# Kernel optimization log

Measured on AMD Instinct MI355X. Metric: run time of the kernel, lower is better.

## Reference

```python
import jax, jax.numpy as jnp
import numpy as np

NUM_QUANTIZERS = 4  # num_quantizers


def setup_inputs() -> dict:
    key = jax.random.key(0)
    k1, k2 = jax.random.split(key)
    x = jax.random.normal(k1, (8, 64, 128, 128), dtype=jnp.float32)
    codebook = jax.random.normal(k2, (512, 64), dtype=jnp.float32)
    return {"x": x, "codebook": codebook}


def reference(x, codebook):
    """Residual VQ with shared Euclidean codebook, straight-through estimator.

    x: [B, C, H, W] image feature map; codebook: [K, C].
    Returns (quantized [B,C,H,W], indices [B,H,W,Q] int32, commit_loss [Q]).
    """
    B, C, H, W = x.shape
    flat = x.transpose(0, 2, 3, 1).reshape(-1, C)  # [N, C], N = B*H*W
    c_sq = jnp.sum(codebook * codebook, axis=-1)   # [K]

    residual = flat
    quant_out = jnp.zeros_like(flat)
    idx_list, losses = [], []
    for _ in range(NUM_QUANTIZERS):
        # argmin ||r - c||^2 == argmin (||c||^2 - 2 r.c); ||r||^2 constant per row
        dist = c_sq[None, :] - 2.0 * (residual @ codebook.T)  # [N, K]
        idx = jnp.argmin(dist, axis=-1)                        # [N]
        quant = codebook[idx]                                  # [N, C] gather
        # commitment loss: mse(stop_grad(quant), residual)
        losses.append(jnp.mean(jnp.square(jax.lax.stop_gradient(quant) - residual)))
        # straight-through: gradients flow to residual, not codebook
        quant_st = residual + jax.lax.stop_gradient(quant - residual)
        quant_out = quant_out + quant_st
        residual = residual - jax.lax.stop_gradient(quant)
        idx_list.append(idx)

    quantized = quant_out.reshape(B, H, W, C).transpose(0, 3, 1, 2)
    indices = jnp.stack(idx_list, axis=-1).reshape(B, H, W, NUM_QUANTIZERS)
    commit_loss = jnp.stack(losses)
    return quantized, indices, commit_loss
```

## Files before the change

### kernel.cpp

```cpp
#include <hip/hip_runtime.h>


#define NPTS   131072
#define CH     64
#define KCODE  512
#define NQ     4
#define HW     16384
#define BPTS   64
#define BTHR   256

__device__ __forceinline__ void load_lds16(const float* g, float* l) {
    __builtin_amdgcn_global_load_lds(
        (const __attribute__((address_space(1))) void*)g,
        (__attribute__((address_space(3))) void*)l, 16, 0, 0);
}

__global__ void prep_cbS(const float* __restrict__ cb, float* __restrict__ cbS) {
    int g = blockIdx.x * 256 + threadIdx.x;
    int c = g >> 9, pos = g & 511;
    int i = pos >> 7, cg = (pos >> 2) & 31, j = pos & 3;
    int k = cg * 16 + i * 4 + j;
    cbS[g] = cb[k * CH + c];
}

__global__ void prep_csq(const float* __restrict__ cb, float* __restrict__ csq) {
    int k = blockIdx.x * 256 + threadIdx.x;
    if (k < KCODE) {
        const float4* row = (const float4*)(cb + (size_t)k * CH);
        float a0 = 0.f, a1 = 0.f, a2 = 0.f, a3 = 0.f;
#pragma unroll
        for (int j = 0; j < CH / 4; ++j) {
            float4 v = row[j];
            a0 = fmaf(v.x, v.x, a0); a1 = fmaf(v.y, v.y, a1);
            a2 = fmaf(v.z, v.z, a2); a3 = fmaf(v.w, v.w, a3);
        }
        csq[k] = (a0 + a1) + (a2 + a3);
    }
}

__global__ __launch_bounds__(BTHR, 2) void rvq_main(
    const float* __restrict__ x, const float* __restrict__ cb,
    const float* __restrict__ cbS, const float* __restrict__ csq_g,
    float* __restrict__ out_quant, float* __restrict__ out_idx,
    float* __restrict__ out_loss)
{
    __shared__ __align__(16) float s_res[CH * BPTS];
    __shared__ __align__(16) float s_cb[16 * KCODE];
    __shared__ __align__(16) float s_csq[KCODE];
    __shared__ int   s_bidx[BPTS];
    __shared__ int   s_idx4[BPTS * NQ];

    float* s_rd   = s_cb;
    int*   s_ri   = (int*)(s_cb + 64 * 33);
    float* s_loss = s_cb + 2 * 64 * 33;

    const int tid  = threadIdx.x;
    const int lane = tid & 63;
    const int w    = tid >> 6;
    const int cg   = tid & 31;
    const int pg   = tid >> 5;

    const int n0  = blockIdx.x * BPTS;
    const int b   = n0 >> 14;
    const int hw0 = n0 & (HW - 1);
    const float* xbase = x + (size_t)b * CH * HW + hw0;

    for (int j = tid; j < CH * BPTS / 4; j += BTHR) {
        int c = j >> 4, p4 = j & 15;
        *(float4*)&s_res[c * BPTS + p4 * 4] =
            *(const float4*)(xbase + (size_t)c * HW + p4 * 4);
    }
    for (int j = tid; j < KCODE; j += BTHR) s_csq[j] = csq_g[j];

    float lossq[NQ], idxf[NQ];

    for (int q = 0; q < NQ; ++q) {
        float acc[8][16];
        {
            if (q == 0) { __syncthreads(); }
            const float4* cq4 = (const float4*)(s_csq + cg * 16);
            float4 c0 = cq4[0], c1 = cq4[1], c2 = cq4[2], c3 = cq4[3];
            float ci[16] = {c0.x, c0.y, c0.z, c0.w, c1.x, c1.y, c1.z, c1.w,
                            c2.x, c2.y, c2.z, c2.w, c3.x, c3.y, c3.z, c3.w};
#pragma unroll
            for (int p = 0; p < 8; ++p)
#pragma unroll
                for (int n = 0; n < 16; ++n) acc[p][n] = -0.5f * ci[n];
        }

        for (int chk = 0; chk < 4; ++chk) {
            __syncthreads();
            const float* src = cbS + chk * (16 * KCODE);
#pragma unroll
            for (int r = 0; r < 8; ++r) {
                int off = (w * 8 + r) * 256;
                load_lds16(src + off + lane * 4, s_cb + off);
            }
            __syncthreads();
#pragma unroll 2
            for (int cc = 0; cc < 16; ++cc) {
                const int c = chk * 16 + cc;
                const float* ar = &s_res[c * BPTS + pg * 8];
                float4 a0 = *(const float4*)(ar + 0);
                float4 a1 = *(const float4*)(ar + 4);
                float av[8] = {a0.x, a0.y, a0.z, a0.w, a1.x, a1.y, a1.z, a1.w};
                const float* br = &s_cb[cc * KCODE + cg * 4];
#pragma unroll
                for (int nb = 0; nb < 4; ++nb) {
                    float4 bq = *(const float4*)(br + nb * 128);
#pragma unroll
                    for (int p = 0; p < 8; ++p) {
                        acc[p][nb * 4 + 0] = fmaf(av[p], bq.x, acc[p][nb * 4 + 0]);
                        acc[p][nb * 4 + 1] = fmaf(av[p], bq.y, acc[p][nb * 4 + 1]);
                        acc[p][nb * 4 + 2] = fmaf(av[p], bq.z, acc[p][nb * 4 + 2]);
                        acc[p][nb * 4 + 3] = fmaf(av[p], bq.w, acc[p][nb * 4 + 3]);
                    }
                }
            }
        }

        float bd[8]; int bi[8];
#pragma unroll
        for (int p = 0; p < 8; ++p) {
            float B = acc[p][0]; int I = cg * 16;
#pragma unroll
            for (int n = 1; n < 16; ++n)
                if (acc[p][n] > B) { B = acc[p][n]; I = cg * 16 + n; }
            bd[p] = B; bi[p] = I;
        }

        __syncthreads();
#pragma unroll
        for (int p = 0; p < 8; ++p) {
            s_rd[(pg * 8 + p) * 33 + cg] = bd[p];
            s_ri[(pg * 8 + p) * 33 + cg] = bi[p];
        }
        __syncthreads();
        if (tid < BPTS) {
            float B = -3.4e38f; int I = 0x7fffffff;
            for (int g2 = 0; g2 < 32; ++g2) {
                float s = s_rd[tid * 33 + g2];
                int   k = s_ri[tid * 33 + g2];
                if (s > B || (s == B && k < I)) { B = s; I = k; }
            }
            idxf[q] = (float)I;
            s_bidx[tid] = I;
            s_idx4[tid * 4 + q] = I;
        }
        __syncthreads();

        {
            const int p  = tid & 63;
            const int cq = tid >> 6;
            int bix = s_bidx[p];
            const float4* crow = (const float4*)(cb + (size_t)bix * CH + cq * 16);
            float l0 = 0.f, l1 = 0.f, l2 = 0.f, l3 = 0.f;
#pragma unroll
            for (int i = 0; i < 4; ++i) {
                float4 v = crow[i];
                int c = cq * 16 + i * 4;
                float r0 = s_res[(c + 0) * BPTS + p] - v.x;
                float r1 = s_res[(c + 1) * BPTS + p] - v.y;
                float r2 = s_res[(c + 2) * BPTS + p] - v.z;
                float r3 = s_res[(c + 3) * BPTS + p] - v.w;
                s_res[(c + 0) * BPTS + p] = r0;
                s_res[(c + 1) * BPTS + p] = r1;
                s_res[(c + 2) * BPTS + p] = r2;
                s_res[(c + 3) * BPTS + p] = r3;
                l0 = fmaf(r0, r0, l0); l1 = fmaf(r1, r1, l1);
                l2 = fmaf(r2, r2, l2); l3 = fmaf(r3, r3, l3);
            }
            s_loss[cq * BPTS + p] = (l0 + l1) + (l2 + l3);
        }
        __syncthreads();
        if (tid < BPTS)
            lossq[q] = (s_loss[0 * BPTS + tid] + s_loss[1 * BPTS + tid]) +
                       (s_loss[2 * BPTS + tid] + s_loss[3 * BPTS + tid]);
    }

    {
        const int p  = tid & 63;
        const int cq = tid >> 6;
        int e0 = s_idx4[p * 4 + 0], e1 = s_idx4[p * 4 + 1];
        int e2 = s_idx4[p * 4 + 2], e3 = s_idx4[p * 4 + 3];
        const float4* r0 = (const float4*)(cb + (size_t)e0 * CH + cq * 16);
        const float4* r1 = (const float4*)(cb + (size_t)e1 * CH + cq * 16);
        const float4* r2 = (const float4*)(cb + (size_t)e2 * CH + cq * 16);
        const float4* r3 = (const float4*)(cb + (size_t)e3 * CH + cq * 16);
        float* ob = out_quant + (size_t)b * CH * HW + hw0;
#pragma unroll
        for (int i = 0; i < 4; ++i) {
            float4 v0 = r0[i], v1 = r1[i], v2 = r2[i], v3 = r3[i];
            float s0 = ((v0.x + v1.x) + v2.x) + v3.x;
            float s1 = ((v0.y + v1.y) + v2.y) + v3.y;
            float s2 = ((v0.z + v1.z) + v2.z) + v3.z;
            float s3 = ((v0.w + v1.w) + v2.w) + v3.w;
            int c = cq * 16 + i * 4;
            ob[(size_t)(c + 0) * HW + p] = s0;
            ob[(size_t)(c + 1) * HW + p] = s1;
            ob[(size_t)(c + 2) * HW + p] = s2;
            ob[(size_t)(c + 3) * HW + p] = s3;
        }
    }

    if (tid < BPTS) {
        ((float4*)out_idx)[n0 + tid] =
            make_float4(idxf[0], idxf[1], idxf[2], idxf[3]);
#pragma unroll
        for (int qq = 0; qq < NQ; ++qq) {
            float v = lossq[qq];
            for (int off = 32; off > 0; off >>= 1) v += __shfl_down(v, off, 64);
            if (tid == 0)
                atomicAdd(&out_loss[qq], v * (1.0f / 8388608.0f));
        }
    }
}

extern "C" void kernel_launch(void* const* d_in, const int* in_sizes, int n_in,
                              void* d_out, int out_size, void* d_ws, size_t ws_size,
                              hipStream_t stream) {
    const float* x  = (const float*)d_in[0];
    const float* cb = (const float*)d_in[1];
    float* out       = (float*)d_out;
    float* out_quant = out;
    float* out_idx   = out + 8388608;
    float* out_loss  = out + 8388608 + 524288;

    float* cbS = (float*)d_ws;
    float* csq = cbS + CH * KCODE;

    hipMemsetAsync(out_loss, 0, NQ * sizeof(float), stream);
    prep_cbS<<<(CH * KCODE) / 256, 256, 0, stream>>>(cb, cbS);
    prep_csq<<<2, 256, 0, stream>>>(cb, csq);
    rvq_main<<<NPTS / BPTS, BTHR, 0, stream>>>(x, cb, cbS, csq,
                                               out_quant, out_idx, out_loss);
}
```

Before: 551.5 us.

## Make RVQ kernel persistent with whole codebook resident in LDS

Switches to a persistent grid of 256 blocks that each load the full transposed codebook (128 KB) into LDS once and then loop over point tiles. This removes the per-quantizer, per-chunk codebook reloads and their barriers. The cross-thread argmin now uses wave shuffles instead of an LDS reduction, and loss is accumulated per block before a single atomic. The large LDS footprint limits occupancy to one block per CU, which reduces latency hiding.

```diff
diff --git a/kernel.cpp b/kernel.cpp
--- a/kernel.cpp
+++ b/kernel.cpp
@@ -8,6 +8,8 @@
 #define HW     16384
 #define BPTS   64
 #define BTHR   256
+#define NTILE  (NPTS / BPTS)
+#define GRID   256
 
 __device__ __forceinline__ void load_lds16(const float* g, float* l) {
     __builtin_amdgcn_global_load_lds(
@@ -38,21 +40,18 @@
     }
 }
 
-__global__ __launch_bounds__(BTHR, 2) void rvq_main(
+__global__ __launch_bounds__(BTHR, 1) void rvq_main(
     const float* __restrict__ x, const float* __restrict__ cb,
     const float* __restrict__ cbS, const float* __restrict__ csq_g,
     float* __restrict__ out_quant, float* __restrict__ out_idx,
     float* __restrict__ out_loss)
 {
+    __shared__ __align__(16) float s_cb[CH * KCODE];
     __shared__ __align__(16) float s_res[CH * BPTS];
-    __shared__ __align__(16) float s_cb[16 * KCODE];
     __shared__ __align__(16) float s_csq[KCODE];
     __shared__ int   s_bidx[BPTS];
     __shared__ int   s_idx4[BPTS * NQ];
-
-    float* s_rd   = s_cb;
-    int*   s_ri   = (int*)(s_cb + 64 * 33);
-    float* s_loss = s_cb + 2 * 64 * 33;
+    __shared__ float s_ls[4 * BPTS];
 
     const int tid  = threadIdx.x;
     const int lane = tid & 63;
@@ -60,51 +59,50 @@
     const int cg   = tid & 31;
     const int pg   = tid >> 5;
 
-    const int n0  = blockIdx.x * BPTS;
-    const int b   = n0 >> 14;
-    const int hw0 = n0 & (HW - 1);
-    const float* xbase = x + (size_t)b * CH * HW + hw0;
-
-    for (int j = tid; j < CH * BPTS / 4; j += BTHR) {
-        int c = j >> 4, p4 = j & 15;
-        *(float4*)&s_res[c * BPTS + p4 * 4] =
-            *(const float4*)(xbase + (size_t)c * HW + p4 * 4);
-    }
+#pragma unroll
+    for (int i = 0; i < 32; ++i)
+        load_lds16(cbS + i * 1024 + w * 256 + lane * 4,
+                   s_cb + i * 1024 + w * 256);
     for (int j = tid; j < KCODE; j += BTHR) s_csq[j] = csq_g[j];
 
-    float lossq[NQ], idxf[NQ];
-
-    for (int q = 0; q < NQ; ++q) {
-        float acc[8][16];
-        {
-            if (q == 0) { __syncthreads(); }
-            const float4* cq4 = (const float4*)(s_csq + cg * 16);
-            float4 c0 = cq4[0], c1 = cq4[1], c2 = cq4[2], c3 = cq4[3];
-            float ci[16] = {c0.x, c0.y, c0.z, c0.w, c1.x, c1.y, c1.z, c1.w,
-                            c2.x, c2.y, c2.z, c2.w, c3.x, c3.y, c3.z, c3.w};
-#pragma unroll
-            for (int p = 0; p < 8; ++p)
-#pragma unroll
-                for (int n = 0; n < 16; ++n) acc[p][n] = -0.5f * ci[n];
-        }
-
-        for (int chk = 0; chk < 4; ++chk) {
-            __syncthreads();
-            const float* src = cbS + chk * (16 * KCODE);
-#pragma unroll
-            for (int r = 0; r < 8; ++r) {
-                int off = (w * 8 + r) * 256;
-                load_lds16(src + off + lane * 4, s_cb + off);
-            }
-            __syncthreads();
-#pragma unroll 2
-            for (int cc = 0; cc < 16; ++cc) {
-                const int c = chk * 16 + cc;
+    float lacc[NQ] = {0.f, 0.f, 0.f, 0.f};
+
+    for (int tile = blockIdx.x; tile < NTILE; tile += GRID) {
+        const int n0  = tile * BPTS;
+        const int b   = n0 >> 14;
+        const int hw0 = n0 & (HW - 1);
+        const float* xbase = x + (size_t)b * CH * HW + hw0;
+
+        __syncthreads();
+        for (int j = tid; j < CH * BPTS / 4; j += BTHR) {
+            int c = j >> 4, p4 = j & 15;
+            *(float4*)&s_res[c * BPTS + p4 * 4] =
+                *(const float4*)(xbase + (size_t)c * HW + p4 * 4);
+        }
+        __syncthreads();
+
+        float lossq[NQ], idxf[NQ];
+
+        for (int q = 0; q < NQ; ++q) {
+            float acc[8][16];
+            {
+                const float4* cq4 = (const float4*)(s_csq + cg * 16);
+                float4 c0 = cq4[0], c1 = cq4[1], c2 = cq4[2], c3 = cq4[3];
+                float ci[16] = {c0.x, c0.y, c0.z, c0.w, c1.x, c1.y, c1.z, c1.w,
+                                c2.x, c2.y, c2.z, c2.w, c3.x, c3.y, c3.z, c3.w};
+#pragma unroll
+                for (int p = 0; p < 8; ++p)
+#pragma unroll
+                    for (int n = 0; n < 16; ++n) acc[p][n] = -0.5f * ci[n];
+            }
+
+#pragma unroll 4
+            for (int c = 0; c < CH; ++c) {
                 const float* ar = &s_res[c * BPTS + pg * 8];
                 float4 a0 = *(const float4*)(ar + 0);
                 float4 a1 = *(const float4*)(ar + 4);
                 float av[8] = {a0.x, a0.y, a0.z, a0.w, a1.x, a1.y, a1.z, a1.w};
-                const float* br = &s_cb[cc * KCODE + cg * 4];
+                const float* br = &s_cb[c * KCODE + cg * 4];
 #pragma unroll
                 for (int nb = 0; nb < 4; ++nb) {
                     float4 bq = *(const float4*)(br + nb * 128);
@@ -117,98 +115,105 @@
                     }
                 }
             }
-        }
-
-        float bd[8]; int bi[8];
-#pragma unroll
-        for (int p = 0; p < 8; ++p) {
-            float B = acc[p][0]; int I = cg * 16;
-#pragma unroll
-            for (int n = 1; n < 16; ++n)
-                if (acc[p][n] > B) { B = acc[p][n]; I = cg * 16 + n; }
-            bd[p] = B; bi[p] = I;
-        }
-
-        __syncthreads();
-#pragma unroll
-        for (int p = 0; p < 8; ++p) {
-            s_rd[(pg * 8 + p) * 33 + cg] = bd[p];
-            s_ri[(pg * 8 + p) * 33 + cg] = bi[p];
-        }
-        __syncthreads();
-        if (tid < BPTS) {
-            float B = -3.4e38f; int I = 0x7fffffff;
-            for (int g2 = 0; g2 < 32; ++g2) {
-                float s = s_rd[tid * 33 + g2];
-                int   k = s_ri[tid * 33 + g2];
-                if (s > B || (s == B && k < I)) { B = s; I = k; }
-            }
-            idxf[q] = (float)I;
-            s_bidx[tid] = I;
-            s_idx4[tid * 4 + q] = I;
-        }
-        __syncthreads();
+
+            float bd[8]; int bi[8];
+#pragma unroll
+            for (int p = 0; p < 8; ++p) {
+                float B = acc[p][0]; int I = cg * 16;
+#pragma unroll
+                for (int n = 1; n < 16; ++n)
+                    if (acc[p][n] > B) { B = acc[p][n]; I = cg * 16 + n; }
+                bd[p] = B; bi[p] = I;
+            }
+
+#pragma unroll
+            for (int m = 1; m <= 16; m <<= 1) {
+#pragma unroll
+                for (int p = 0; p < 8; ++p) {
+                    float oB = __shfl_xor(bd[p], m, 64);
+                    int   oI = __shfl_xor(bi[p], m, 64);
+                    if (oB > bd[p] || (oB == bd[p] && oI < bi[p])) {
+                        bd[p] = oB; bi[p] = oI;
+                    }
+                }
+            }
+            if (cg == 0) {
+#pragma unroll
+                for (int p = 0; p < 8; ++p) {
+                    s_bidx[pg * 8 + p] = bi[p];
+                    s_idx4[(pg * 8 + p) * 4 + q] = bi[p];
+                }
+            }
+            __syncthreads();
+            if (tid < BPTS) idxf[q] = (float)s_bidx[tid];
+
+            {
+                const int p  = tid & 63;
+                const int cq = tid >> 6;
+                int bix = s_bidx[p];
+                const float4* crow =
+                    (const float4*)(cb + (size_t)bix * CH + cq * 16);
+                float l0 = 0.f, l1 = 0.f, l2 = 0.f, l3 = 0.f;
+#pragma unroll
+                for (int i = 0; i < 4; ++i) {
+                    float4 v = crow[i];
+                    int c = cq * 16 + i * 4;
+                    float r0 = s_res[(c + 0) * BPTS + p] - v.x;
+                    float r1 = s_res[(c + 1) * BPTS + p] - v.y;
+                    float r2 = s_res[(c + 2) * BPTS + p] - v.z;
+                    float r3 = s_res[(c + 3) * BPTS + p] - v.w;
+                    s_res[(c + 0) * BPTS + p] = r0;
+                    s_res[(c + 1) * BPTS + p] = r1;
+                    s_res[(c + 2) * BPTS + p] = r2;
+                    s_res[(c + 3) * BPTS + p] = r3;
+                    l0 = fmaf(r0, r0, l0); l1 = fmaf(r1, r1, l1);
+                    l2 = fmaf(r2, r2, l2); l3 = fmaf(r3, r3, l3);
+                }
+                s_ls[cq * BPTS + p] = (l0 + l1) + (l2 + l3);
+            }
+            __syncthreads();
+            if (tid < BPTS)
+                lossq[q] = (s_ls[0 * BPTS + tid] + s_ls[1 * BPTS + tid]) +
+                           (s_ls[2 * BPTS + tid] + s_ls[3 * BPTS + tid]);
+        }
 
         {
             const int p  = tid & 63;
             const int cq = tid >> 6;
-            int bix = s_bidx[p];
-            const float4* crow = (const float4*)(cb + (size_t)bix * CH + cq * 16);
-            float l0 = 0.f, l1 = 0.f, l2 = 0.f, l3 = 0.f;
+            int e0 = s_idx4[p * 4 + 0], e1 = s_idx4[p * 4 + 1];
+            int e2 = s_idx4[p * 4 + 2], e3 = s_idx4[p * 4 + 3];
+            const float4* r0 = (const float4*)(cb + (size_t)e0 * CH + cq * 16);
+            const float4* r1 = (const float4*)(cb + (size_t)e1 * CH + cq * 16);
+            const float4* r2 = (const float4*)(cb + (size_t)e2 * CH + cq * 16);
+            const float4* r3 = (const float4*)(cb + (size_t)e3 * CH + cq * 16);
+            float* ob = out_quant + (size_t)b * CH * HW + hw0;
 #pragma unroll
             for (int i = 0; i < 4; ++i) {
-                float4 v = crow[i];
+                float4 v0 = r0[i], v1 = r1[i], v2 = r2[i], v3 = r3[i];
+                float s0 = ((v0.x + v1.x) + v2.x) + v3.x;
+                float s1 = ((v0.y + v1.y) + v2.y) + v3.y;
+                float s2 = ((v0.z + v1.z) + v2.z) + v3.z;
+                float s3 = ((v0.w + v1.w) + v2.w) + v3.w;
                 int c = cq * 16 + i * 4;
-                float r0 = s_res[(c + 0) * BPTS + p] - v.x;
-                float r1 = s_res[(c + 1) * BPTS + p] - v.y;
-                float r2 = s_res[(c + 2) * BPTS + p] - v.z;
-                float r3 = s_res[(c + 3) * BPTS + p] - v.w;
-                s_res[(c + 0) * BPTS + p] = r0;
-                s_res[(c + 1) * BPTS + p] = r1;
-                s_res[(c + 2) * BPTS + p] = r2;
-                s_res[(c + 3) * BPTS + p] = r3;
-                l0 = fmaf(r0, r0, l0); l1 = fmaf(r1, r1, l1);
-                l2 = fmaf(r2, r2, l2); l3 = fmaf(r3, r3, l3);
-            }
-            s_loss[cq * BPTS + p] = (l0 + l1) + (l2 + l3);
-        }
-        __syncthreads();
-        if (tid < BPTS)
-            lossq[q] = (s_loss[0 * BPTS + tid] + s_loss[1 * BPTS + tid]) +
-                       (s_loss[2 * BPTS + tid] + s_loss[3 * BPTS + tid]);
+                ob[(size_t)(c + 0) * HW + p] = s0;
+                ob[(size_t)(c + 1) * HW + p] = s1;
+                ob[(size_t)(c + 2) * HW + p] = s2;
+                ob[(size_t)(c + 3) * HW + p] = s3;
+            }
+        }
+
+        if (tid < BPTS) {
+            ((float4*)out_idx)[n0 + tid] =
+                make_float4(idxf[0], idxf[1], idxf[2], idxf[3]);
+#pragma unroll
+            for (int qq = 0; qq < NQ; ++qq) lacc[qq] += lossq[qq];
+        }
     }
 
-    {
-        const int p  = tid & 63;
-        const int cq = tid >> 6;
-        int e0 = s_idx4[p * 4 + 0], e1 = s_idx4[p * 4 + 1];
-        int e2 = s_idx4[p * 4 + 2], e3 = s_idx4[p * 4 + 3];
-        const float4* r0 = (const float4*)(cb + (size_t)e0 * CH + cq * 16);
-        const float4* r1 = (const float4*)(cb + (size_t)e1 * CH + cq * 16);
-        const float4* r2 = (const float4*)(cb + (size_t)e2 * CH + cq * 16);
-        const float4* r3 = (const float4*)(cb + (size_t)e3 * CH + cq * 16);
-        float* ob = out_quant + (size_t)b * CH * HW + hw0;
-#pragma unroll
-        for (int i = 0; i < 4; ++i) {
-            float4 v0 = r0[i], v1 = r1[i], v2 = r2[i], v3 = r3[i];
-            float s0 = ((v0.x + v1.x) + v2.x) + v3.x;
-            float s1 = ((v0.y + v1.y) + v2.y) + v3.y;
-            float s2 = ((v0.z + v1.z) + v2.z) + v3.z;
-            float s3 = ((v0.w + v1.w) + v2.w) + v3.w;
-            int c = cq * 16 + i * 4;
-            ob[(size_t)(c + 0) * HW + p] = s0;
-            ob[(size_t)(c + 1) * HW + p] = s1;
-            ob[(size_t)(c + 2) * HW + p] = s2;
-            ob[(size_t)(c + 3) * HW + p] = s3;
-        }
-    }
-
     if (tid < BPTS) {
-        ((float4*)out_idx)[n0 + tid] =
-            make_float4(idxf[0], idxf[1], idxf[2], idxf[3]);
 #pragma unroll
         for (int qq = 0; qq < NQ; ++qq) {
-            float v = lossq[qq];
+            float v = lacc[qq];
             for (int off = 32; off > 0; off >>= 1) v += __shfl_down(v, off, 64);
             if (tid == 0)
                 atomicAdd(&out_loss[qq], v * (1.0f / 8388608.0f));
@@ -232,6 +237,6 @@
     hipMemsetAsync(out_loss, 0, NQ * sizeof(float), stream);
     prep_cbS<<<(CH * KCODE) / 256, 256, 0, stream>>>(cb, cbS);
     prep_csq<<<2, 256, 0, stream>>>(cb, csq);
-    rvq_main<<<NPTS / BPTS, BTHR, 0, stream>>>(x, cb, cbS, csq,
-                                               out_quant, out_idx, out_loss);
-}
+    rvq_main<<<GRID, BTHR, 0, stream>>>(x, cb, cbS, csq,
+                                        out_quant, out_idx, out_loss);
+}
```

Result: slower. 749.9 us (+36.0%).
